# Kernel optimization log

Hardware: AMD Instinct MI355X
Metric: run time of the kernel (lower is better)

## Reference

```python
import jax, jax.numpy as jnp
import numpy as np

D = 1024
H = 16
HD = D // H
B = 2
T = 2048


def _rope_tables(t, hd):
    inv_freq = 1.0 / (10000.0 ** (np.arange(0, hd, 2, dtype=np.float32) / hd))
    ang = np.arange(t, dtype=np.float32)[:, None] * inv_freq[None, :]  # [T, hd/2]
    emb = np.concatenate([ang, ang], axis=-1)  # [T, hd]
    return jnp.asarray(np.cos(emb)), jnp.asarray(np.sin(emb))


def setup_inputs() -> dict:
    key = jax.random.key(0)
    kx, kq, kk, kv, ko = jax.random.split(key, 5)
    scale = 0.02
    x = jax.random.normal(kx, (B, T, D), dtype=jnp.float32)
    cos, sin = _rope_tables(T, HD)
    mask = jnp.tril(jnp.ones((T, T), dtype=jnp.int32))[None, None]  # [1,1,T,T]
    wq = jax.random.normal(kq, (D, D), dtype=jnp.float32) * scale
    wk = jax.random.normal(kk, (D, D), dtype=jnp.float32) * scale
    wv = jax.random.normal(kv, (D, D), dtype=jnp.float32) * scale
    wo = jax.random.normal(ko, (D, D), dtype=jnp.float32) * scale
    return {"x": x, "cos": cos, "sin": sin, "mask": mask,
            "wq": wq, "wk": wk, "wv": wv, "wo": wo}


def _rotate_half(t):
    t1, t2 = jnp.split(t, 2, axis=-1)
    return jnp.concatenate((-t2, t1), axis=-1)


def reference(x, cos, sin, mask, wq, wk, wv, wo):
    Bx, Tx, C = x.shape
    hd = C // H
    # nn.Linear: y = x @ W.T  -> [B,T,H,hd] -> [B,H,T,hd]
    q = (x @ wq.T).reshape(Bx, Tx, H, hd).transpose(0, 2, 1, 3)
    k = (x @ wk.T).reshape(Bx, Tx, H, hd).transpose(0, 2, 1, 3)
    v = (x @ wv.T).reshape(Bx, Tx, H, hd).transpose(0, 2, 1, 3)
    c = cos[:Tx][None, None]  # [1,1,T,hd]
    s = sin[:Tx][None, None]
    q = q * c + _rotate_half(q) * s
    k = k * c + _rotate_half(k) * s
    att = jnp.einsum('bhqd,bhkd->bhqk', q, k) * (hd ** -0.5)
    att = jnp.where(mask[:, :, :Tx, :Tx] == 0, -jnp.inf, att)
    att = jax.nn.softmax(att, axis=-1)
    out = jnp.einsum('bhqk,bhkd->bhqd', att, v)
    out = out.transpose(0, 2, 1, 3).reshape(Bx, Tx, C)
    return out @ wo.T
```

## Files before the change

### kernel.cpp

```cpp
#include <hip/hip_runtime.h>
#include <math.h>

constexpr int D  = 1024;
constexpr int H  = 16;
constexpr int HD = 64;
constexpr int B  = 2;
constexpr int T  = 2048;
constexpr int M  = B * T;

constexpr size_t XSZ = (size_t)M * D;
constexpr size_t WSZ = (size_t)D * D;

typedef float  f32x4   __attribute__((ext_vector_type(4)));
typedef float  f32x16  __attribute__((ext_vector_type(16)));
typedef __bf16 bf16x8  __attribute__((ext_vector_type(8)));
typedef __bf16 bf16x4  __attribute__((ext_vector_type(4)));
typedef unsigned u32x2 __attribute__((ext_vector_type(2)));
typedef unsigned u32x4 __attribute__((ext_vector_type(4)));

static __device__ inline f32x4 mfma16(bf16x8 a, bf16x8 b, f32x4 c) {
  return __builtin_amdgcn_mfma_f32_16x16x32_bf16(a, b, c, 0, 0, 0);
}
static __device__ inline f32x16 mfma32(bf16x8 a, bf16x8 b, f32x16 c) {
  return __builtin_amdgcn_mfma_f32_32x32x16_bf16(a, b, c, 0, 0, 0);
}
static __device__ inline unsigned cvtpk(float a, float b) {
  unsigned r;
  asm("v_cvt_pk_bf16_f32 %0, %1, %2" : "=v"(r) : "v"(a), "v"(b));
  return r;
}
static __device__ inline u32x2 plswap(unsigned a, unsigned b) {
  return __builtin_amdgcn_permlane32_swap(a, b, false, false);
}
static __device__ inline void gload16(const __bf16* g, __bf16* l) {
  __builtin_amdgcn_global_load_lds(
      (const __attribute__((address_space(1))) void*)g,
      (__attribute__((address_space(3))) void*)l, 16, 0, 0);
}

__global__ __launch_bounds__(256)
void cvt_all(const float* __restrict__ x, const float* __restrict__ wq,
             const float* __restrict__ wk, const float* __restrict__ wv,
             const float* __restrict__ wo, __bf16* __restrict__ out) {
  size_t idx = ((size_t)blockIdx.x * 256 + threadIdx.x) * 8;
  const float* src;
  if      (idx < XSZ)            src = x  + idx;
  else if (idx < XSZ + WSZ)      src = wq + (idx - XSZ);
  else if (idx < XSZ + 2 * WSZ)  src = wk + (idx - XSZ - WSZ);
  else if (idx < XSZ + 3 * WSZ)  src = wv + (idx - XSZ - 2 * WSZ);
  else                           src = wo + (idx - XSZ - 3 * WSZ);
  float4 a = *reinterpret_cast<const float4*>(src);
  float4 b = *reinterpret_cast<const float4*>(src + 4);
  bf16x8 o;
  o[0] = (__bf16)a.x; o[1] = (__bf16)a.y; o[2] = (__bf16)a.z; o[3] = (__bf16)a.w;
  o[4] = (__bf16)b.x; o[5] = (__bf16)b.y; o[6] = (__bf16)b.z; o[7] = (__bf16)b.w;
  *reinterpret_cast<bf16x8*>(out + idx) = o;
}

template<int MODE>
__global__ __launch_bounds__(512)
void gemm_mfma(const __bf16* __restrict__ A,
               const __bf16* __restrict__ W0, const __bf16* __restrict__ W1,
               const __bf16* __restrict__ W2,
               const float* __restrict__ cosT, const float* __restrict__ sinT,
               void* __restrict__ out0, void* __restrict__ out1,
               void* __restrict__ out2) {
  __shared__ __bf16 As[128 * 64];
  __shared__ __bf16 Bs[128 * 64];

  const int tid  = threadIdx.x;
  const int lane = tid & 63;
  const int w    = tid >> 6;
  const int wm   = w >> 1;
  const int wn   = w & 1;
  const int l15  = lane & 15, lg = lane >> 4;
  const int m0   = blockIdx.y * 128;

  int which, n0;
  const __bf16* Bw;
  if (MODE == 1) {
    which = blockIdx.x >> 3;
    n0 = (blockIdx.x & 7) * 128;
    Bw = which == 0 ? W0 : which == 1 ? W1 : W2;
  } else {
    which = 0;
    n0 = blockIdx.x * 128;
    Bw = W0;
  }

  f32x4 acc[2][4];
  #pragma unroll
  for (int i = 0; i < 2; ++i)
    #pragma unroll
    for (int j = 0; j < 4; ++j) acc[i][j] = (f32x4){0.f, 0.f, 0.f, 0.f};

  const int e0 = tid * 8;
  const int r0 = e0 >> 6;
  const int c0 = e0 & 63;

  for (int k0 = 0; k0 < 1024; k0 += 64) {
    const __bf16* ga = A  + (size_t)(m0 + r0) * 1024 + k0 + c0;
    const __bf16* gb = Bw + (size_t)(n0 + r0) * 1024 + k0 + c0;
    gload16(ga,             As + e0);
    gload16(ga + 64 * 1024, As + e0 + 4096);
    gload16(gb,             Bs + e0);
    gload16(gb + 64 * 1024, Bs + e0 + 4096);
    __syncthreads();

    #pragma unroll
    for (int ks = 0; ks < 2; ++ks) {
      bf16x8 af[2], bfr[4];
      #pragma unroll
      for (int mt = 0; mt < 2; ++mt)
        af[mt] = *reinterpret_cast<const bf16x8*>(
            &As[(wm * 32 + mt * 16 + l15) * 64 + ks * 32 + lg * 8]);
      #pragma unroll
      for (int nt = 0; nt < 4; ++nt)
        bfr[nt] = *reinterpret_cast<const bf16x8*>(
            &Bs[(wn * 64 + nt * 16 + l15) * 64 + ks * 32 + lg * 8]);
      #pragma unroll
      for (int mt = 0; mt < 2; ++mt)
        #pragma unroll
        for (int nt = 0; nt < 4; ++nt)
          acc[mt][nt] = mfma16(af[mt], bfr[nt], acc[mt][nt]);
    }
    __syncthreads();
  }

  if (MODE == 0) {
    float* o = (float*)out0;
    #pragma unroll
    for (int mt = 0; mt < 2; ++mt) {
      const int mb = m0 + wm * 32 + mt * 16 + lg * 4;
      #pragma unroll
      for (int nt = 0; nt < 4; ++nt) {
        const int n = n0 + wn * 64 + nt * 16 + l15;
        #pragma unroll
        for (int r = 0; r < 4; ++r)
          o[(size_t)(mb + r) * 1024 + n] = acc[mt][nt][r];
      }
    }
  } else if (which < 2) {
    __bf16* dst = which == 0 ? (__bf16*)out0 : (__bf16*)out1;
    const float qs = (which == 0) ? 0.180336880f : 1.0f;
    const int h = (n0 + wn * 64) >> 6;
    #pragma unroll
    for (int mt = 0; mt < 2; ++mt) {
      const int tb   = m0 + wm * 32 + mt * 16 + lg * 4;
      const int bb   = tb >> 11;
      const int tloc = tb & 2047;
      #pragma unroll
      for (int r = 0; r < 4; ++r) {
        const int t = tloc + r;
        #pragma unroll
        for (int nt = 0; nt < 2; ++nt) {
          const int hd = nt * 16 + l15;
          const float c = cosT[t * HD + hd];
          const float s = sinT[t * HD + hd];
          const float v1 = acc[mt][nt][r];
          const float v2 = acc[mt][nt + 2][r];
          const size_t base = (((size_t)(bb * H + h)) * T + t) * HD;
          dst[base + hd]      = (__bf16)((v1 * c - v2 * s) * qs);
          dst[base + hd + 32] = (__bf16)((v2 * c + v1 * s) * qs);
        }
      }
    }
  } else {
    __bf16* dst = (__bf16*)out2;
    const int h = (n0 + wn * 64) >> 6;
    #pragma unroll
    for (int mt = 0; mt < 2; ++mt) {
      const int tb = m0 + wm * 32 + mt * 16 + lg * 4;
      const int bb = tb >> 11;
      const int t0 = tb & 2047;
      #pragma unroll
      for (int nt = 0; nt < 4; ++nt) {
        const int hd = nt * 16 + l15;
        bf16x4 ov;
        #pragma unroll
        for (int r = 0; r < 4; ++r) ov[r] = (__bf16)acc[mt][nt][r];
        *reinterpret_cast<bf16x4*>(
            &dst[(((size_t)(bb * H + h)) * HD + hd) * T + t0]) = ov;
      }
    }
  }
}

__global__ __launch_bounds__(256, 2)
void attn_v8(const __bf16* __restrict__ Q, const __bf16* __restrict__ K,
             const __bf16* __restrict__ Vt, __bf16* __restrict__ Ob) {
  const int tid  = threadIdx.x;
  const int lane = tid & 63;
  const int w    = tid >> 6;
  const int l31  = lane & 31;
  const int hi   = lane >> 5;
  const int x    = blockIdx.x;
  const int bh   = blockIdx.y;

  const int wi = (bh < 16) ? w : (w ^ 1);
  const int qt = (wi == 0) ? 2 * x : (wi == 1) ? 63 - 2 * x
               : (wi == 2) ? 2 * x + 1 : 62 - 2 * x;
  const int q0w    = qt * 32;
  const int ntiles = qt + 1;

  const __bf16* Qg = Q  + (size_t)bh * T * HD;
  const __bf16* Kg = K  + (size_t)bh * T * HD;
  const __bf16* Vg = Vt + (size_t)bh * HD * T;

  bf16x8 qfr[4];
  #pragma unroll
  for (int st = 0; st < 4; ++st)
    qfr[st] = *reinterpret_cast<const bf16x8*>(
        Qg + (size_t)(q0w + l31) * HD + st * 16 + hi * 8);

  float m_run = -INFINITY, l_run = 0.f;
  f32x16 oacc0, oacc1;
  #pragma unroll
  for (int i = 0; i < 16; ++i) { oacc0[i] = 0.f; oacc1[i] = 0.f; }

  const __bf16* kbase = Kg + (size_t)l31 * HD + hi * 8;
  const __bf16* vbase = Vg + (size_t)l31 * T + hi * 8;

#define LOADKV(K0, K1, K2, K3, V00, V01, V10, V11, jj)                        \
  do {                                                                        \
    const __bf16* _kp = kbase + (size_t)(jj) * 32 * HD;                       \
    K0 = *reinterpret_cast<const bf16x8*>(_kp);                               \
    K1 = *reinterpret_cast<const bf16x8*>(_kp + 16);                          \
    K2 = *reinterpret_cast<const bf16x8*>(_kp + 32);                          \
    K3 = *reinterpret_cast<const bf16x8*>(_kp + 48);                          \
    const __bf16* _vp = vbase + (size_t)(jj) * 32;                            \
    V00 = *reinterpret_cast<const bf16x8*>(_vp);                              \
    V01 = *reinterpret_cast<const bf16x8*>(_vp + 16);                         \
    V10 = *reinterpret_cast<const bf16x8*>(_vp + (size_t)32 * T);             \
    V11 = *reinterpret_cast<const bf16x8*>(_vp + (size_t)32 * T + 16);        \
  } while (0)

#define TILE(K0, K1, K2, K3, V00, V01, V10, V11, jj)                          \
  do {                                                                        \
    f32x16 sva, svb;                                                          \
    _Pragma("unroll")                                                         \
    for (int _i = 0; _i < 16; ++_i) { sva[_i] = 0.f; svb[_i] = 0.f; }         \
    sva = mfma32(K0, qfr[0], sva);                                            \
    svb = mfma32(K1, qfr[1], svb);                                            \
    sva = mfma32(K2, qfr[2], sva);                                            \
    svb = mfma32(K3, qfr[3], svb);                                            \
    f32x16 sv;                                                                \
    _Pragma("unroll")                                                         \
    for (int _i = 0; _i < 16; ++_i) sv[_i] = sva[_i] + svb[_i];               \
    if ((jj) == qt) {                         \
      const int _q = q0w + l31;                                               \
      const int _kb = (jj) * 32 + 4 * hi;                                     \
      _Pragma("unroll")                                                       \
      for (int _r = 0; _r < 16; ++_r) {                                       \
        const int _key = _kb + (_r & 3) + 8 * (_r >> 2);                      \
        if (_key > _q) sv[_r] = -INFINITY;                                    \
      }                                                                       \
    }                                                                         \
    float _mx[8];                                                             \
    _Pragma("unroll")                                                         \
    for (int _i = 0; _i < 8; ++_i) _mx[_i] = fmaxf(sv[_i], sv[_i + 8]);       \
    _Pragma("unroll")                                                         \
    for (int _s = 4; _s > 0; _s >>= 1)                                        \
      _Pragma("unroll")                                                       \
      for (int _i = 0; _i < 4; ++_i)                                          \
        if (_i < _s) _mx[_i] = fmaxf(_mx[_i], _mx[_i + _s]);                  \
    union { float f; unsigned u; } _cv; _cv.f = _mx[0];                       \
    u32x2 _sw = plswap(_cv.u, _cv.u);                                         \
    union { unsigned u; float f; } _c0, _c1; _c0.u = _sw[0]; _c1.u = _sw[1];  \
    const float _pmax = fmaxf(_c0.f, _c1.f);                                  \
    if (__any(_pmax > m_run + 8.f)) {                                         \
      const float _mn = fmaxf(m_run, _pmax);                                  \
      const float _rs = exp2f(m_run - _mn);                                   \
      l_run *= _rs;                                                           \
      _Pragma("unroll")                                                       \
      for (int _i = 0; _i < 16; ++_i) { oacc0[_i] *= _rs; oacc1[_i] *= _rs; } \
      m_run = _mn;                                                            \
    }                                                                         \
    _Pragma("unroll")                                                         \
    for (int _i = 0; _i < 16; ++_i) sv[_i] = exp2f(sv[_i] - m_run);           \
    float _sm[8];                                                             \
    _Pragma("unroll")                                                         \
    for (int _i = 0; _i < 8; ++_i) _sm[_i] = sv[_i] + sv[_i + 8];             \
    _Pragma("unroll")                                                         \
    for (int _s = 4; _s > 0; _s >>= 1)                                        \
      _Pragma("unroll")                                                       \
      for (int _i = 0; _i < 4; ++_i)                                          \
        if (_i < _s) _sm[_i] += _sm[_i + _s];                                 \
    l_run += _sm[0];                                                          \
    unsigned _cp[8];                                                          \
    _Pragma("unroll")                                                         \
    for (int _m = 0; _m < 4; ++_m) {                                          \
      _cp[2 * _m]     = cvtpk(sv[4 * _m],     sv[4 * _m + 1]);                \
      _cp[2 * _m + 1] = cvtpk(sv[4 * _m + 2], sv[4 * _m + 3]);                \
    }                                                                         \
    {                                                                         \
      u32x2 _r0 = plswap(_cp[0], _cp[2]);                                     \
      u32x2 _r1 = plswap(_cp[1], _cp[3]);                                     \
      union { u32x4 u; bf16x8 v; } _pu;                                       \
      _pu.u = (u32x4){_r0[0], _r1[0], _r0[1], _r1[1]};                        \
      oacc0 = mfma32(V00, _pu.v, oacc0);                                      \
      oacc1 = mfma32(V10, _pu.v, oacc1);                                      \
    }                                                                         \
    {                                                                         \
      u32x2 _r0 = plswap(_cp[4], _cp[6]);                                     \
      u32x2 _r1 = plswap(_cp[5], _cp[7]);                                     \
      union { u32x4 u; bf16x8 v; } _pu;                                       \
      _pu.u = (u32x4){_r0[0], _r1[0], _r0[1], _r1[1]};                        \
      oacc0 = mfma32(V01, _pu.v, oacc0);                                      \
      oacc1 = mfma32(V11, _pu.v, oacc1);                                      \
    }                                                                         \
  } while (0)

  bf16x8 kA0, kA1, kA2, kA3, vA00, vA01, vA10, vA11;
  bf16x8 kB0, kB1, kB2, kB3, vB00, vB01, vB10, vB11;

  LOADKV(kA0, kA1, kA2, kA3, vA00, vA01, vA10, vA11, 0);
  int j = 0;
  #pragma unroll 1
  for (;;) {
    if (j + 1 < ntiles)
      LOADKV(kB0, kB1, kB2, kB3, vB00, vB01, vB10, vB11, j + 1);
    TILE(kA0, kA1, kA2, kA3, vA00, vA01, vA10, vA11, j);
    if (j + 1 >= ntiles) break;
    if (j + 2 < ntiles)
      LOADKV(kA0, kA1, kA2, kA3, vA00, vA01, vA10, vA11, j + 2);
    TILE(kB0, kB1, kB2, kB3, vB00, vB01, vB10, vB11, j + 1);
    if (j + 2 >= ntiles) break;
    j += 2;
  }
#undef TILE
#undef LOADKV

  const float l_tot = l_run + __shfl_xor(l_run, 32);
  const float inv = 1.f / l_tot;
  const int b = bh >> 4, h = bh & 15;
  const int q_abs = q0w + l31;
  const size_t rowbase = ((size_t)(b * T + q_abs)) * 1024 + h * 64;
  #pragma unroll
  for (int rg = 0; rg < 4; ++rg) {
    bf16x4 o0, o1;
    #pragma unroll
    for (int r = 0; r < 4; ++r) {
      o0[r] = (__bf16)(oacc0[rg * 4 + r] * inv);
      o1[r] = (__bf16)(oacc1[rg * 4 + r] * inv);
    }
    *reinterpret_cast<bf16x4*>(&Ob[rowbase + rg * 8 + hi * 4])      = o0;
    *reinterpret_cast<bf16x4*>(&Ob[rowbase + 32 + rg * 8 + hi * 4]) = o1;
  }
}

extern "C" void kernel_launch(void* const* d_in, const int* in_sizes, int n_in,
                              void* d_out, int out_size, void* d_ws, size_t ws_size,
                              hipStream_t stream) {
  const float* x    = (const float*)d_in[0];
  const float* cosT = (const float*)d_in[1];
  const float* sinT = (const float*)d_in[2];
  const float* wq   = (const float*)d_in[4];
  const float* wk   = (const float*)d_in[5];
  const float* wv   = (const float*)d_in[6];
  const float* wo   = (const float*)d_in[7];
  float* out = (float*)d_out;

  __bf16* xb   = (__bf16*)d_ws;
  __bf16* wqb  = xb  + XSZ;
  __bf16* wkb  = wqb + WSZ;
  __bf16* wvb  = wkb + WSZ;
  __bf16* wob  = wvb + WSZ;
  __bf16* Qh   = wob + WSZ;
  __bf16* Kh   = Qh  + XSZ;
  __bf16* Vth  = Kh  + XSZ;
  __bf16* attb = Vth + XSZ;

  cvt_all<<<(XSZ + 4 * WSZ) / 8 / 256, 256, 0, stream>>>(x, wq, wk, wv, wo, xb);

  gemm_mfma<1><<<dim3(24, 32), 512, 0, stream>>>(
      xb, wqb, wkb, wvb, cosT, sinT, Qh, Kh, Vth);

  attn_v8<<<dim3(16, 32), 256, 0, stream>>>(Qh, Kh, Vth, attb);

  gemm_mfma<0><<<dim3(8, 32), 512, 0, stream>>>(
      attb, wob, nullptr, nullptr, nullptr, nullptr, out, nullptr, nullptr);
}
```

Measured before the change: 154.6 us.

## Split attention KV loop across wave pairs with LDS softmax merge

Each 32-row query tile is now processed by two waves that take alternating KV tiles (even and odd). Their partial output accumulators and running max and sum are merged through shared memory with a flash-decoding-style rescale. The grid becomes 1024 one-dimensional blocks, each covering two query tiles (a short one paired with a long one), and the launch-bounds occupancy hint rises from 2 to 4 blocks. The goal is to shorten the per-wave critical path and increase parallelism across the GPU, at the cost of a __syncthreads, added LDS traffic and extra merge arithmetic.

```diff
diff --git a/kernel.cpp b/kernel.cpp
--- a/kernel.cpp
+++ b/kernel.cpp
@@ -186,22 +186,27 @@
   }
 }
 
-__global__ __launch_bounds__(256, 2)
-void attn_v8(const __bf16* __restrict__ Q, const __bf16* __restrict__ K,
-             const __bf16* __restrict__ Vt, __bf16* __restrict__ Ob) {
+__global__ __launch_bounds__(256, 4)
+void attn_v10(const __bf16* __restrict__ Q, const __bf16* __restrict__ K,
+              const __bf16* __restrict__ Vt, __bf16* __restrict__ Ob) {
+  __shared__ float Mrg[2][64][34];
+
   const int tid  = threadIdx.x;
   const int lane = tid & 63;
   const int w    = tid >> 6;
   const int l31  = lane & 31;
   const int hi   = lane >> 5;
-  const int x    = blockIdx.x;
-  const int bh   = blockIdx.y;
-
-  const int wi = (bh < 16) ? w : (w ^ 1);
-  const int qt = (wi == 0) ? 2 * x : (wi == 1) ? 63 - 2 * x
-               : (wi == 2) ? 2 * x + 1 : 62 - 2 * x;
-  const int q0w    = qt * 32;
-  const int ntiles = qt + 1;
+
+  const int id = blockIdx.x;
+  const int r  = id >> 8;
+  const int c  = id & 255;
+  const int bh = (c & 7) + 8 * r;
+  const int v  = c >> 3;
+
+  const int J  = (w >> 1) ^ (r & 1);
+  const int wp = w & 1;
+  const int qt = (J == 0) ? v : 63 - v;
+  const int q0w = qt * 32;
 
   const __bf16* Qg = Q  + (size_t)bh * T * HD;
   const __bf16* Kg = K  + (size_t)bh * T * HD;
@@ -314,38 +319,59 @@
   bf16x8 kA0, kA1, kA2, kA3, vA00, vA01, vA10, vA11;
   bf16x8 kB0, kB1, kB2, kB3, vB00, vB01, vB10, vB11;
 
-  LOADKV(kA0, kA1, kA2, kA3, vA00, vA01, vA10, vA11, 0);
-  int j = 0;
-  #pragma unroll 1
-  for (;;) {
-    if (j + 1 < ntiles)
-      LOADKV(kB0, kB1, kB2, kB3, vB00, vB01, vB10, vB11, j + 1);
-    TILE(kA0, kA1, kA2, kA3, vA00, vA01, vA10, vA11, j);
-    if (j + 1 >= ntiles) break;
-    if (j + 2 < ntiles)
-      LOADKV(kA0, kA1, kA2, kA3, vA00, vA01, vA10, vA11, j + 2);
-    TILE(kB0, kB1, kB2, kB3, vB00, vB01, vB10, vB11, j + 1);
-    if (j + 2 >= ntiles) break;
-    j += 2;
+  int jj = wp;
+  if (jj <= qt) {
+    LOADKV(kA0, kA1, kA2, kA3, vA00, vA01, vA10, vA11, jj);
+    #pragma unroll 1
+    for (;;) {
+      if (jj + 2 <= qt)
+        LOADKV(kB0, kB1, kB2, kB3, vB00, vB01, vB10, vB11, jj + 2);
+      TILE(kA0, kA1, kA2, kA3, vA00, vA01, vA10, vA11, jj);
+      if (jj + 2 > qt) break;
+      if (jj + 4 <= qt)
+        LOADKV(kA0, kA1, kA2, kA3, vA00, vA01, vA10, vA11, jj + 4);
+      TILE(kB0, kB1, kB2, kB3, vB00, vB01, vB10, vB11, jj + 2);
+      if (jj + 4 > qt) break;
+      jj += 4;
+    }
   }
 #undef TILE
 #undef LOADKV
 
-  const float l_tot = l_run + __shfl_xor(l_run, 32);
-  const float inv = 1.f / l_tot;
-  const int b = bh >> 4, h = bh & 15;
-  const int q_abs = q0w + l31;
-  const size_t rowbase = ((size_t)(b * T + q_abs)) * 1024 + h * 64;
-  #pragma unroll
-  for (int rg = 0; rg < 4; ++rg) {
-    bf16x4 o0, o1;
-    #pragma unroll
-    for (int r = 0; r < 4; ++r) {
-      o0[r] = (__bf16)(oacc0[rg * 4 + r] * inv);
-      o1[r] = (__bf16)(oacc1[rg * 4 + r] * inv);
-    }
-    *reinterpret_cast<bf16x4*>(&Ob[rowbase + rg * 8 + hi * 4])      = o0;
-    *reinterpret_cast<bf16x4*>(&Ob[rowbase + 32 + rg * 8 + hi * 4]) = o1;
+  float* row = &Mrg[J][lane][0];
+  if (wp == 1) {
+    #pragma unroll
+    for (int i = 0; i < 16; ++i) row[i]      = oacc0[i];
+    #pragma unroll
+    for (int i = 0; i < 16; ++i) row[16 + i] = oacc1[i];
+    row[32] = m_run;
+    row[33] = l_run;
+  }
+  __syncthreads();
+  if (wp == 0) {
+    const float mB = row[32], lB = row[33];
+    const float mS = fmaxf(m_run, mB);
+    const float sA = exp2f(m_run - mS);
+    const float sB = exp2f(mB - mS);
+    float l_lane = l_run * sA + lB * sB;
+    const float l_tot = l_lane + __shfl_xor(l_lane, 32);
+    const float inv = 1.f / l_tot;
+
+    const int b = bh >> 4, h = bh & 15;
+    const int q_abs = q0w + l31;
+    const size_t rowbase = ((size_t)(b * T + q_abs)) * 1024 + h * 64;
+    #pragma unroll
+    for (int rg = 0; rg < 4; ++rg) {
+      bf16x4 o0, o1;
+      #pragma unroll
+      for (int rr = 0; rr < 4; ++rr) {
+        const int i = rg * 4 + rr;
+        o0[rr] = (__bf16)((oacc0[i] * sA + row[i]      * sB) * inv);
+        o1[rr] = (__bf16)((oacc1[i] * sA + row[16 + i] * sB) * inv);
+      }
+      *reinterpret_cast<bf16x4*>(&Ob[rowbase + rg * 8 + hi * 4])      = o0;
+      *reinterpret_cast<bf16x4*>(&Ob[rowbase + 32 + rg * 8 + hi * 4]) = o1;
+    }
   }
 }
 
@@ -376,7 +402,7 @@
   gemm_mfma<1><<<dim3(24, 32), 512, 0, stream>>>(
       xb, wqb, wkb, wvb, cosT, sinT, Qh, Kh, Vth);
 
-  attn_v8<<<dim3(16, 32), 256, 0, stream>>>(Qh, Kh, Vth, attb);
+  attn_v10<<<dim3(1024), 256, 0, stream>>>(Qh, Kh, Vth, attb);
 
   gemm_mfma<0><<<dim3(8, 32), 512, 0, stream>>>(
       attb, wob, nullptr, nullptr, nullptr, nullptr, out, nullptr, nullptr);
```

After: 204.9 us. +32.6%, slower.
